# Performance work log

Measured on AMD Instinct MI355X. Metric: run time of the kernel, lower is better.

## Reference

```python
import jax, jax.numpy as jnp
import numpy as np

HEADS = 8
HEAD_DIM = 64
SCALE = HEAD_DIM ** -0.5


def setup_inputs() -> dict:
    key = jax.random.key(0)
    k1, k2, k3 = jax.random.split(key, 3)
    b, p, n, dim = 8, 16, 256, 384
    inner = HEADS * HEAD_DIM  # 512
    x = jax.random.normal(k1, (b, p, n, dim), dtype=jnp.float32)
    w_qkv = jax.random.normal(k2, (dim, 3 * inner), dtype=jnp.float32) * (dim ** -0.5)
    w_out = jax.random.normal(k3, (inner, dim), dtype=jnp.float32) * (inner ** -0.5)
    b_out = jnp.zeros((dim,), dtype=jnp.float32)
    return {"x": x, "w_qkv": w_qkv, "w_out": w_out, "b_out": b_out}


def reference(x, w_qkv, w_out, b_out):
    b, p, n, dim = x.shape
    inner = HEADS * HEAD_DIM
    qkv = jnp.einsum('bpnd,de->bpne', x, w_qkv)  # [b,p,n,3*inner]
    q, k, v = jnp.split(qkv, 3, axis=-1)
    # [b,p,n,inner] -> [b,p,h,n,hd]
    def to_heads(t):
        return t.reshape(b, p, n, HEADS, HEAD_DIM).transpose(0, 1, 3, 2, 4)
    q, k, v = to_heads(q), to_heads(k), to_heads(v)
    dots = jnp.einsum('bphqd,bphkd->bphqk', q, k) * SCALE
    attn = jax.nn.softmax(dots, axis=-1)
    out = jnp.einsum('bphqk,bphkd->bphqd', attn, v)
    out = out.transpose(0, 1, 3, 2, 4).reshape(b, p, n, inner)
    return jnp.einsum('bpni,id->bpnd', out, w_out) + b_out
```

## Files before the change

### kernel.cpp

```cpp
#include <hip/hip_runtime.h>
#include <stdint.h>

#define DEVFN __device__ __forceinline__

typedef __attribute__((ext_vector_type(8))) __bf16 bf16x8;
typedef __attribute__((ext_vector_type(8))) short short8;
typedef __attribute__((ext_vector_type(4))) float f32x4;

DEVFN unsigned short f2bf(float f) {
  union { float f; unsigned u; } v; v.f = f;
  return (unsigned short)((v.u + 0x7FFFu + ((v.u >> 16) & 1u)) >> 16);
}

DEVFN void gload_lds16(const void* g, void* l) {
  __builtin_amdgcn_global_load_lds(
      (const __attribute__((address_space(1))) void*)(uintptr_t)g,
      (__attribute__((address_space(3))) void*)(uint32_t)(uintptr_t)l,
      16, 0, 0);
}


__global__ void k_cast_x(const float* __restrict__ x, short* __restrict__ xb, int n8) {
  int i = blockIdx.x * blockDim.x + threadIdx.x;
  if (i >= n8) return;
  const f32x4* xf = (const f32x4*)x;
  f32x4 a = xf[2 * i], b = xf[2 * i + 1];
  short8 s;
  s[0] = (short)f2bf(a[0]); s[1] = (short)f2bf(a[1]);
  s[2] = (short)f2bf(a[2]); s[3] = (short)f2bf(a[3]);
  s[4] = (short)f2bf(b[0]); s[5] = (short)f2bf(b[1]);
  s[6] = (short)f2bf(b[2]); s[7] = (short)f2bf(b[3]);
  ((short8*)xb)[i] = s;
}

__global__ void k_transpose_bf(const float* __restrict__ w, short* __restrict__ wt, int R, int C) {
  int i = blockIdx.x * blockDim.x + threadIdx.x;
  if (i >= R * C) return;
  int c = i / R, r = i - c * R;
  wt[i] = (short)f2bf(w[(size_t)r * C + c]);
}


template <int BF16_OUT, int NB>
__global__ __launch_bounds__(256, NB == 8 ? 2 : 3)
void k_gemm(const short* __restrict__ A, const short* __restrict__ Bt,
            unsigned short* __restrict__ Cb, float* __restrict__ Cf,
            const float* __restrict__ bias, int M, int N, int K) {
  constexpr int BN = NB * 32;
  constexpr int BCH = NB / 2;
  __shared__ short As[3][128 * 32];
  __shared__ short Bs[3][BN * 32];
  const int tid = threadIdx.x;
  const int l = tid & 63, w = tid >> 6;
  const int ntile = N / BN;
  const int nwg = gridDim.x, cpx = nwg >> 3;
  const int bid = (blockIdx.x & 7) * cpx + (blockIdx.x >> 3);
  const int mt = bid / ntile, nt = bid % ntile;
  const int m0 = mt << 7, n0 = nt * BN;
  const int wm = (w >> 1) << 6, wn = (w & 1) * (NB * 16);

  f32x4 acc[4][NB];
#pragma unroll
  for (int i = 0; i < 4; i++)
#pragma unroll
    for (int j = 0; j < NB; j++) acc[i][j] = (f32x4){0.f, 0.f, 0.f, 0.f};

  const int nsteps = K >> 5;

  auto stage = [&](int buf, int t) {
#pragma unroll
    for (int c = 0; c < 2; ++c) {
      int ch = tid + c * 256;
      int row = ch >> 2;
      int sl = (ch & 3) ^ ((row >> 1) & 3);
      gload_lds16(A + (size_t)(m0 + row) * K + t * 32 + sl * 8, &As[buf][ch * 8]);
    }
#pragma unroll
    for (int c = 0; c < BCH; ++c) {
      int ch = tid + c * 256;
      int row = ch >> 2;
      int sl = (ch & 3) ^ ((row >> 1) & 3);
      gload_lds16(Bt + (size_t)(n0 + row) * K + t * 32 + sl * 8, &Bs[buf][ch * 8]);
    }
  };
  const int sp8 = (((l >> 4) ^ ((l >> 1) & 3)) << 3);
  auto compute = [&](int buf) {
    bf16x8 af[4], bfr[NB];
#pragma unroll
    for (int i = 0; i < 4; i++)
      af[i] = *(const bf16x8*)&As[buf][(wm + i * 16 + (l & 15)) * 32 + sp8];
#pragma unroll
    for (int j = 0; j < NB; j++)
      bfr[j] = *(const bf16x8*)&Bs[buf][(wn + j * 16 + (l & 15)) * 32 + sp8];
#pragma unroll
    for (int i = 0; i < 4; i++)
#pragma unroll
      for (int j = 0; j < NB; j++)
        acc[i][j] = __builtin_amdgcn_mfma_f32_16x16x32_bf16(af[i], bfr[j], acc[i][j], 0, 0, 0);
  };

  stage(0, 0);
  stage(1, 1);
#pragma unroll 1
  for (int t = 0; t < nsteps; ++t) {
    if (t + 1 < nsteps) {
      if constexpr (NB == 8)
        asm volatile("s_waitcnt vmcnt(6)" ::: "memory");
      else
        asm volatile("s_waitcnt vmcnt(4)" ::: "memory");
    } else {
      asm volatile("s_waitcnt vmcnt(0)" ::: "memory");
    }
    __builtin_amdgcn_sched_barrier(0);
    __builtin_amdgcn_s_barrier();
    __builtin_amdgcn_sched_barrier(0);
    if (t + 2 < nsteps) stage((t + 2) % 3, t + 2);
    compute(t % 3);
  }

#pragma unroll
  for (int i = 0; i < 4; i++) {
    int mrow = m0 + wm + i * 16 + ((l >> 4) << 2);
#pragma unroll
    for (int j = 0; j < NB; j++) {
      int ncol = n0 + wn + j * 16 + (l & 15);
#pragma unroll
      for (int r = 0; r < 4; r++) {
        if (BF16_OUT) {
          Cb[(size_t)(mrow + r) * N + ncol] = f2bf(acc[i][j][r]);
        } else {
          Cf[(size_t)(mrow + r) * N + ncol] = acc[i][j][r] + bias[ncol];
        }
      }
    }
  }
}


__global__ __launch_bounds__(512, 2)
void k_attn(const short* __restrict__ qkv, unsigned short* __restrict__ O) {
  __shared__ short Kl[256 * 64];
  __shared__ short Vt[64 * 256];
  __shared__ short Pc[8][16 * 40];

  const int tid = threadIdx.x, l = tid & 63, w = tid >> 6;
  const int bh = blockIdx.x;
  const int bp = bh >> 3, h = bh & 7;
  const size_t tokbase = (size_t)bp * 256 * 1536;
  const int qoff = h * 64, koff = 512 + h * 64, voff = 1024 + h * 64;

#pragma unroll
  for (int c = 0; c < 4; ++c) {
    int ch = tid + c * 512;
    int row = ch >> 3, s = ch & 7;
    int sg = s ^ (row & 7);
    gload_lds16(qkv + tokbase + (size_t)row * 1536 + koff + sg * 8, &Kl[ch * 8]);
  }
#pragma unroll
  for (int c = 0; c < 4; ++c) {
    int ch = tid + c * 512;
    int row = ch >> 3, d0 = (ch & 7) * 8;
    short8 v = *(const short8*)(qkv + tokbase + (size_t)row * 1536 + voff + d0);
#pragma unroll
    for (int j = 0; j < 8; ++j) {
      int d = d0 + j;
      Vt[d * 256 + (((((row >> 3) ^ (d & 15))) << 3) | (row & 7))] = v[j];
    }
  }
  __syncthreads();

  const float CEXP = 0.125f * 1.44269504f;

#pragma unroll 1
  for (int it = 0; it < 2; ++it) {
    const int q0 = w * 32 + it * 16;
    bf16x8 qa[2];
#pragma unroll
    for (int dc = 0; dc < 2; ++dc)
      qa[dc] = *(const bf16x8*)(qkv + tokbase + (size_t)(q0 + (l & 15)) * 1536 + qoff +
                                dc * 32 + (l >> 4) * 8);
    f32x4 s[16];
#pragma unroll
    for (int kt = 0; kt < 16; kt++) s[kt] = (f32x4){0.f, 0.f, 0.f, 0.f};
#pragma unroll
    for (int dc = 0; dc < 2; ++dc) {
#pragma unroll
      for (int kt = 0; kt < 16; ++kt) {
        int kcol = kt * 16 + (l & 15);
        int sl = (dc * 4 + (l >> 4)) ^ (kcol & 7);
        bf16x8 kb = *(const bf16x8*)&Kl[kcol * 64 + sl * 8];
        s[kt] = __builtin_amdgcn_mfma_f32_16x16x32_bf16(qa[dc], kb, s[kt], 0, 0, 0);
      }
    }
    float rs[4];
#pragma unroll
    for (int r = 0; r < 4; ++r) {
      float m = s[0][r];
#pragma unroll
      for (int kt = 1; kt < 16; kt++) m = fmaxf(m, s[kt][r]);
      for (int off = 1; off < 16; off <<= 1) m = fmaxf(m, __shfl_xor(m, off, 64));
      float sum = 0.f;
#pragma unroll
      for (int kt = 0; kt < 16; kt++) {
        float p = exp2f((s[kt][r] - m) * CEXP);
        s[kt][r] = p;
        sum += p;
      }
      for (int off = 1; off < 16; off <<= 1) sum += __shfl_xor(sum, off, 64);
      rs[r] = 1.0f / sum;
    }
    f32x4 o[4];
#pragma unroll
    for (int dt = 0; dt < 4; dt++) o[dt] = (f32x4){0.f, 0.f, 0.f, 0.f};
    short* pc = &Pc[w][0];
#pragma unroll
    for (int kc = 0; kc < 8; ++kc) {
#pragma unroll
      for (int t2 = 0; t2 < 2; ++t2) {
        int kt = kc * 2 + t2;
#pragma unroll
        for (int r = 0; r < 4; ++r)
          pc[((l >> 4) * 4 + r) * 40 + t2 * 16 + (l & 15)] = (short)f2bf(s[kt][r]);
      }
      asm volatile("" ::: "memory");
      bf16x8 pa = *(const bf16x8*)&pc[(l & 15) * 40 + (l >> 4) * 8];
#pragma unroll
      for (int dt = 0; dt < 4; ++dt) {
        int d = dt * 16 + (l & 15);
        int sl = (kc * 4 + (l >> 4)) ^ (d & 15);
        bf16x8 vb = *(const bf16x8*)&Vt[d * 256 + sl * 8];
        o[dt] = __builtin_amdgcn_mfma_f32_16x16x32_bf16(pa, vb, o[dt], 0, 0, 0);
      }
      asm volatile("" ::: "memory");
    }
#pragma unroll
    for (int dt = 0; dt < 4; dt++) {
#pragma unroll
      for (int r = 0; r < 4; r++) {
        int qrow = q0 + ((l >> 4) << 2) + r;
        int d = dt * 16 + (l & 15);
        O[(size_t)(bp * 256 + qrow) * 512 + h * 64 + d] = f2bf(o[dt][r] * rs[r]);
      }
    }
  }
}


extern "C" void kernel_launch(void* const* d_in, const int* in_sizes, int n_in,
                              void* d_out, int out_size, void* d_ws, size_t ws_size,
                              hipStream_t stream) {
  const float* x    = (const float*)d_in[0];
  const float* wqkv = (const float*)d_in[1];
  const float* wout = (const float*)d_in[2];
  const float* bout = (const float*)d_in[3];
  float* out = (float*)d_out;
  char* ws = (char*)d_ws;

  short* Wot = (short*)(ws);
  short* Xb  = (short*)(ws + 393216);
  short* Wqt = (short*)(ws + 25559040);
  unsigned short* O = (unsigned short*)(ws + 393216);
  short* QKV = (short*)(ws + 33947648);

  k_cast_x<<<6144, 256, 0, stream>>>(x, Xb, 1572864);
  k_transpose_bf<<<2304, 256, 0, stream>>>(wqkv, Wqt, 384, 1536);
  k_transpose_bf<<<768, 256, 0, stream>>>(wout, Wot, 512, 384);
  k_gemm<1, 8><<<1536, 256, 0, stream>>>(Xb, Wqt, (unsigned short*)QKV, nullptr, nullptr,
                                         32768, 1536, 384);
  k_attn<<<1024, 512, 0, stream>>>(QKV, O);
  k_gemm<0, 4><<<768, 256, 0, stream>>>((const short*)O, Wot, nullptr, out, bout,
                                        32768, 384, 512);
  (void)in_sizes; (void)n_in; (void)out_size; (void)ws_size;
}
```

Baseline: 143.1 us.

## Compute transposed scores so P feeds PV MFMA from registers without LDS

Swaps the MFMA operands for QK^T so each lane holds the scores of a single query column. Softmax then reduces within the lane plus two cross-lane shuffles instead of per-row 16-lane shuffles. The bf16 probabilities are packed directly into the A operand for the PV MFMA, which removes the per-wave LDS staging buffer and its stores and loads. The V transpose into LDS is permuted so its k ordering matches the register-packed P layout, and the reciprocal row sums are redistributed with shuffles at output time.

```diff
diff --git a/kernel.cpp b/kernel.cpp
--- a/kernel.cpp
+++ b/kernel.cpp
@@ -141,9 +141,9 @@
 void k_attn(const short* __restrict__ qkv, unsigned short* __restrict__ O) {
   __shared__ short Kl[256 * 64];
   __shared__ short Vt[64 * 256];
-  __shared__ short Pc[8][16 * 40];
 
   const int tid = threadIdx.x, l = tid & 63, w = tid >> 6;
+  const int g = (l >> 4) & 3;
   const int bh = blockIdx.x;
   const int bp = bh >> 3, h = bh & 7;
   const size_t tokbase = (size_t)bp * 256 * 1536;
@@ -161,10 +161,14 @@
     int ch = tid + c * 512;
     int row = ch >> 3, d0 = (ch & 7) * 8;
     short8 v = *(const short8*)(qkv + tokbase + (size_t)row * 1536 + voff + d0);
+    int kc = row >> 5, u = row & 31;
+    int gg = (u >> 2) & 3;
+    int off = ((u & 16) ? 4 : 0) + (u & 3);
 #pragma unroll
     for (int j = 0; j < 8; ++j) {
       int d = d0 + j;
-      Vt[d * 256 + (((((row >> 3) ^ (d & 15))) << 3) | (row & 7))] = v[j];
+      int sl = (kc * 4 + gg) ^ (d & 15);
+      Vt[d * 256 + sl * 8 + off] = v[j];
     }
   }
   __syncthreads();
@@ -189,57 +193,62 @@
         int kcol = kt * 16 + (l & 15);
         int sl = (dc * 4 + (l >> 4)) ^ (kcol & 7);
         bf16x8 kb = *(const bf16x8*)&Kl[kcol * 64 + sl * 8];
-        s[kt] = __builtin_amdgcn_mfma_f32_16x16x32_bf16(qa[dc], kb, s[kt], 0, 0, 0);
-      }
-    }
-    float rs[4];
-#pragma unroll
-    for (int r = 0; r < 4; ++r) {
-      float m = s[0][r];
-#pragma unroll
-      for (int kt = 1; kt < 16; kt++) m = fmaxf(m, s[kt][r]);
-      for (int off = 1; off < 16; off <<= 1) m = fmaxf(m, __shfl_xor(m, off, 64));
-      float sum = 0.f;
-#pragma unroll
-      for (int kt = 0; kt < 16; kt++) {
-        float p = exp2f((s[kt][r] - m) * CEXP);
+        s[kt] = __builtin_amdgcn_mfma_f32_16x16x32_bf16(kb, qa[dc], s[kt], 0, 0, 0);
+      }
+    }
+    float mx = s[0][0];
+#pragma unroll
+    for (int kt = 0; kt < 16; kt++)
+#pragma unroll
+      for (int r = 0; r < 4; r++) mx = fmaxf(mx, s[kt][r]);
+    mx = fmaxf(mx, __shfl_xor(mx, 16, 64));
+    mx = fmaxf(mx, __shfl_xor(mx, 32, 64));
+    float sum = 0.f;
+#pragma unroll
+    for (int kt = 0; kt < 16; kt++)
+#pragma unroll
+      for (int r = 0; r < 4; r++) {
+        float p = exp2f((s[kt][r] - mx) * CEXP);
         s[kt][r] = p;
         sum += p;
       }
-      for (int off = 1; off < 16; off <<= 1) sum += __shfl_xor(sum, off, 64);
-      rs[r] = 1.0f / sum;
-    }
+    sum += __shfl_xor(sum, 16, 64);
+    sum += __shfl_xor(sum, 32, 64);
+    float rs = 1.0f / sum;
+
     f32x4 o[4];
 #pragma unroll
     for (int dt = 0; dt < 4; dt++) o[dt] = (f32x4){0.f, 0.f, 0.f, 0.f};
-    short* pc = &Pc[w][0];
 #pragma unroll
     for (int kc = 0; kc < 8; ++kc) {
-#pragma unroll
-      for (int t2 = 0; t2 < 2; ++t2) {
-        int kt = kc * 2 + t2;
-#pragma unroll
-        for (int r = 0; r < 4; ++r)
-          pc[((l >> 4) * 4 + r) * 40 + t2 * 16 + (l & 15)] = (short)f2bf(s[kt][r]);
-      }
-      asm volatile("" ::: "memory");
-      bf16x8 pa = *(const bf16x8*)&pc[(l & 15) * 40 + (l >> 4) * 8];
+      union { short8 s8; bf16x8 bf; } pk;
+      pk.s8[0] = (short)f2bf(s[2 * kc][0]);
+      pk.s8[1] = (short)f2bf(s[2 * kc][1]);
+      pk.s8[2] = (short)f2bf(s[2 * kc][2]);
+      pk.s8[3] = (short)f2bf(s[2 * kc][3]);
+      pk.s8[4] = (short)f2bf(s[2 * kc + 1][0]);
+      pk.s8[5] = (short)f2bf(s[2 * kc + 1][1]);
+      pk.s8[6] = (short)f2bf(s[2 * kc + 1][2]);
+      pk.s8[7] = (short)f2bf(s[2 * kc + 1][3]);
 #pragma unroll
       for (int dt = 0; dt < 4; ++dt) {
         int d = dt * 16 + (l & 15);
-        int sl = (kc * 4 + (l >> 4)) ^ (d & 15);
+        int sl = (kc * 4 + g) ^ (d & 15);
         bf16x8 vb = *(const bf16x8*)&Vt[d * 256 + sl * 8];
-        o[dt] = __builtin_amdgcn_mfma_f32_16x16x32_bf16(pa, vb, o[dt], 0, 0, 0);
-      }
-      asm volatile("" ::: "memory");
-    }
+        o[dt] = __builtin_amdgcn_mfma_f32_16x16x32_bf16(pk.bf, vb, o[dt], 0, 0, 0);
+      }
+    }
+    float rsq[4];
+#pragma unroll
+    for (int r = 0; r < 4; ++r)
+      rsq[r] = __shfl(rs, (l & 48) | (g * 4 + r), 64);
 #pragma unroll
     for (int dt = 0; dt < 4; dt++) {
 #pragma unroll
       for (int r = 0; r < 4; r++) {
-        int qrow = q0 + ((l >> 4) << 2) + r;
+        int qrow = q0 + g * 4 + r;
         int d = dt * 16 + (l & 15);
-        O[(size_t)(bp * 256 + qrow) * 512 + h * 64 + d] = f2bf(o[dt][r] * rs[r]);
+        O[(size_t)(bp * 256 + qrow) * 512 + h * 64 + d] = f2bf(o[dt][r] * rsq[r]);
       }
     }
   }
```

Measured after the change: 244.7 us. 1.71x slower.
